# Performance work log

Hardware: AMD Instinct MI355X
Metric: run time of the kernel (lower is better)

Reference implementation:

```python
import jax, jax.numpy as jnp
import numpy as np

NUM_HEADS = 8


def setup_inputs() -> dict:
    key = jax.random.key(0)
    ks = jax.random.split(key, 7)
    b, t, prompt_dim, emb_dim = 2, 4096, 256, 512
    hidden = emb_dim  # head_dim=None -> hidden_dim = emb_dim
    def xavier(k, fan_in, fan_out):
        limit = np.sqrt(6.0 / (fan_in + fan_out)).astype(np.float32)
        return jax.random.uniform(k, (fan_in, fan_out), jnp.float32, -limit, limit)
    return {
        "prompt": jax.random.normal(ks[0], (b, t, prompt_dim), jnp.float32),
        "Wp": xavier(ks[1], prompt_dim, emb_dim),
        "bp": jnp.zeros((emb_dim,), jnp.float32),
        "Wqkv": xavier(ks[2], emb_dim, 3 * hidden),
        "bqkv": jnp.zeros((3 * hidden,), jnp.float32),
        "Wo": xavier(ks[3], hidden, prompt_dim),
        "bo": jnp.zeros((prompt_dim,), jnp.float32),
    }


def reference(prompt, Wp, bp, Wqkv, bqkv, Wo, bo):
    # prompt_proj
    x = prompt @ Wp + bp                      # [b, t, emb_dim]
    b, t, c = x.shape
    qkv = x @ Wqkv + bqkv                     # [b, t, 3*hidden]
    q, k, v = jnp.split(qkv, 3, axis=2)
    def to_heads(z):
        return z.reshape(b, t, NUM_HEADS, -1).transpose(0, 2, 1, 3)  # [b, h, t, d]
    q, k, v = to_heads(q), to_heads(k), to_heads(v)
    d = k.shape[-1]
    scores = jnp.einsum("bhid,bhjd->bhij", q, k) / jnp.sqrt(jnp.float32(d))
    attn = jax.nn.softmax(scores, axis=-1)    # dropout = identity (eval)
    out = jnp.einsum("bhij,bhjd->bhid", attn, v)
    out = out.transpose(0, 2, 1, 3).reshape(b, t, -1)  # [b, t, hidden]
    return out @ Wo + bo                      # [b, t, prompt_dim]
```

## Files before the change

### kernel.cpp

```cpp
#include <hip/hip_runtime.h>
#include <math.h>
#include <stdint.h>


typedef unsigned short u16;
typedef __attribute__((ext_vector_type(8))) __bf16 bf16x8;
typedef __attribute__((ext_vector_type(4))) __bf16 bf16x4;
typedef __attribute__((ext_vector_type(4))) float f32x4;

#define AS1 __attribute__((address_space(1)))
#define AS3 __attribute__((address_space(3)))

__device__ __forceinline__ void async16(const void* g, void* l) {
  __builtin_amdgcn_global_load_lds((const AS1 void*)g, (AS3 void*)l, 16, 0, 0);
}

__device__ __forceinline__ u16 f2bf(float f) {
  union { float f; unsigned u; } c; c.f = f;
  return (u16)((c.u + 0x7fffu + ((c.u >> 16) & 1u)) >> 16);
}

__global__ void prep_kernel(const float* __restrict__ prompt, u16* __restrict__ pbf,
                            const float* __restrict__ Wp, const float* __restrict__ Wqkv,
                            const float* __restrict__ Wo, u16* __restrict__ woT,
                            const float* __restrict__ bp, const float* __restrict__ bqkv,
                            float* __restrict__ bfused, u16* __restrict__ wfT) {
  __shared__ u16 Asf[64 * 40];
  __shared__ u16 Bsf[64 * 32];
  __shared__ float red[256];
  const int bid = blockIdx.x, tid = threadIdx.x;
  if (bid < 96) {
    const int k0 = (bid & 3) * 64, n0 = (bid >> 2) * 64;
    const int lane = tid & 63, w = tid >> 6;
    const int wr = w >> 1, wc = w & 1;
    const int lr = lane >> 4, lc = lane & 15;
    f32x4 acc[2][2];
#pragma unroll
    for (int a = 0; a < 2; a++)
#pragma unroll
      for (int b = 0; b < 2; b++) acc[a][b] = (f32x4){0.f, 0.f, 0.f, 0.f};
    for (int e0 = 0; e0 < 512; e0 += 32) {
      {
        const int er = tid >> 3, ng = (tid & 7) * 8;
        float4 v1 = *(const float4*)&Wqkv[(e0 + er) * 1536 + n0 + ng];
        float4 v2 = *(const float4*)&Wqkv[(e0 + er) * 1536 + n0 + ng + 4];
        Asf[(ng + 0) * 40 + er] = f2bf(v1.x); Asf[(ng + 1) * 40 + er] = f2bf(v1.y);
        Asf[(ng + 2) * 40 + er] = f2bf(v1.z); Asf[(ng + 3) * 40 + er] = f2bf(v1.w);
        Asf[(ng + 4) * 40 + er] = f2bf(v2.x); Asf[(ng + 5) * 40 + er] = f2bf(v2.y);
        Asf[(ng + 6) * 40 + er] = f2bf(v2.z); Asf[(ng + 7) * 40 + er] = f2bf(v2.w);
      }
      {
        const int kr = tid >> 2, ec = (tid & 3) * 8;
        float4 w1 = *(const float4*)&Wp[(k0 + kr) * 512 + e0 + ec];
        float4 w2 = *(const float4*)&Wp[(k0 + kr) * 512 + e0 + ec + 4];
        u16 tmp[8] = {f2bf(w1.x), f2bf(w1.y), f2bf(w1.z), f2bf(w1.w),
                      f2bf(w2.x), f2bf(w2.y), f2bf(w2.z), f2bf(w2.w)};
        *(uint4*)&Bsf[kr * 32 + ec] = *(const uint4*)&tmp[0];
      }
      __syncthreads();
      bf16x8 af[2], bf2[2];
#pragma unroll
      for (int mi = 0; mi < 2; mi++)
        af[mi] = *(const bf16x8*)&Asf[(wr * 32 + mi * 16 + lc) * 40 + lr * 8];
#pragma unroll
      for (int nj = 0; nj < 2; nj++)
        bf2[nj] = *(const bf16x8*)&Bsf[(wc * 32 + nj * 16 + lc) * 32 + lr * 8];
#pragma unroll
      for (int mi = 0; mi < 2; mi++)
#pragma unroll
        for (int nj = 0; nj < 2; nj++)
          acc[mi][nj] = __builtin_amdgcn_mfma_f32_16x16x32_bf16(af[mi], bf2[nj], acc[mi][nj], 0, 0, 0);
      __syncthreads();
    }
#pragma unroll
    for (int mi = 0; mi < 2; mi++)
#pragma unroll
      for (int nj = 0; nj < 2; nj++)
#pragma unroll
        for (int r = 0; r < 4; r++)
          wfT[(n0 + wr * 32 + mi * 16 + 4 * lr + r) * 256 + k0 + wc * 32 + nj * 16 + lc] =
              f2bf(acc[mi][nj][r]);
  } else if (bid < 120) {
    const int nloc = tid & 63, slice = tid >> 6;
    const int n = (bid - 96) * 64 + nloc;
    float s = 0.f;
#pragma unroll 8
    for (int e = slice * 128; e < slice * 128 + 128; e++) s += bp[e] * Wqkv[e * 1536 + n];
    red[tid] = s;
    __syncthreads();
    if (slice == 0)
      bfused[n] = red[nloc] + red[64 + nloc] + red[128 + nloc] + red[192 + nloc] + bqkv[n];
  } else if (bid < 632) {
    int j = (bid - 120) * 256 + tid;
    int n = j >> 9, k = j & 511;
    woT[j] = f2bf(Wo[k * 256 + n]);
  } else {
    int i = (bid - 632) * 256 + tid;
    float4 v = ((const float4*)prompt)[i];
    ushort4 o;
    o.x = f2bf(v.x); o.y = f2bf(v.y); o.z = f2bf(v.z); o.w = f2bf(v.w);
    ((ushort4*)pbf)[i] = o;
  }
}

__global__ __launch_bounds__(256) void gemm_qkv(
    const u16* __restrict__ A, const u16* __restrict__ Bt, const float* __restrict__ bias,
    u16* __restrict__ qO, u16* __restrict__ kO, u16* __restrict__ vO, int K) {
  constexpr int TM = 128, MI = 4, NJ = 4;
  __shared__ __align__(16) u16 As[2][TM * 32];
  __shared__ __align__(16) u16 Bs[2][TM * 32];
  const int tid = threadIdx.x;
  const int lane = tid & 63, w = tid >> 6;
  const int wr = w >> 1, wc = w & 1;
  const int lr = lane >> 4, lc = lane & 15;
  const long tileM = (long)blockIdx.y * 128;
  const long tileN = (long)blockIdx.x * 128;

  f32x4 acc[MI][NJ];
#pragma unroll
  for (int a = 0; a < MI; a++)
#pragma unroll
    for (int b = 0; b < NJ; b++) acc[a][b] = (f32x4){0.f, 0.f, 0.f, 0.f};

  const int r0 = lane >> 2;
  const int blk = lane & 3;

  auto stage = [&](int buf, int k0) {
#pragma unroll
    for (int i = 0; i < 2; i++) {
      int r = w * 32 + i * 16 + r0;
      int g = (blk ^ ((r >> 1) & 3)) << 3;
      async16(A + (tileM + r) * (long)K + k0 + g, (void*)&As[buf][(w * 32 + i * 16) * 32]);
      async16(Bt + (tileN + r) * (long)K + k0 + g, (void*)&Bs[buf][(w * 32 + i * 16) * 32]);
    }
  };

  stage(0, 0);
  for (int k0 = 0; k0 < K; k0 += 32) {
    const int cur = (k0 >> 5) & 1;
    stage(cur ^ 1, (k0 + 32 < K) ? k0 + 32 : 0);
    asm volatile("s_waitcnt vmcnt(4)" ::: "memory");
    asm volatile("s_barrier" ::: "memory");

    bf16x8 af[MI], bfv[NJ];
#pragma unroll
    for (int mi = 0; mi < MI; mi++) {
      int r = wr * 64 + mi * 16 + lc;
      af[mi] = *(const bf16x8*)&As[cur][r * 32 + ((lr ^ ((r >> 1) & 3)) << 3)];
    }
#pragma unroll
    for (int nj = 0; nj < NJ; nj++) {
      int r = wc * 64 + nj * 16 + lc;
      bfv[nj] = *(const bf16x8*)&Bs[cur][r * 32 + ((lr ^ ((r >> 1) & 3)) << 3)];
    }
#pragma unroll
    for (int mi = 0; mi < MI; mi++)
#pragma unroll
      for (int nj = 0; nj < NJ; nj++)
        acc[mi][nj] = __builtin_amdgcn_mfma_f32_16x16x32_bf16(af[mi], bfv[nj], acc[mi][nj], 0, 0, 0);
    asm volatile("s_barrier" ::: "memory");
  }

#pragma unroll
  for (int mi = 0; mi < MI; mi++)
#pragma unroll
    for (int nj = 0; nj < NJ; nj++) {
      long col = tileN + wc * 64 + nj * 16 + lc;
      float bcol = bias[col];
      long row0 = tileM + wr * 64 + mi * 16 + lr * 4;
      int sec = (int)(col >> 9);
      int c2 = (int)(col & 511);
      int h = c2 >> 6, d = c2 & 63;
      long pl = (row0 >> 12) * 8 + h;
      long t0 = row0 & 4095;
      if (sec == 2) {
        ushort4 pk;
        pk.x = f2bf(acc[mi][nj][0] + bcol);
        pk.y = f2bf(acc[mi][nj][1] + bcol);
        pk.z = f2bf(acc[mi][nj][2] + bcol);
        pk.w = f2bf(acc[mi][nj][3] + bcol);
        *(ushort4*)&vO[(pl * 64 + d) * 4096 + t0] = pk;
      } else {
        u16* dst = sec ? kO : qO;
        const float sc = sec ? 1.f : 0.18033688f;
#pragma unroll
        for (int r = 0; r < 4; r++)
          dst[((pl * 4096 + t0 + r) << 6) + d] = f2bf((acc[mi][nj][r] + bcol) * sc);
      }
    }
}

__global__ __launch_bounds__(512) void flash_attn(
    const u16* __restrict__ Q, const u16* __restrict__ Kg,
    const u16* __restrict__ VTg, u16* __restrict__ Op, float* __restrict__ lp) {
  __shared__ __align__(16) u16 KV[2][8192];
  __shared__ __align__(16) u16 Ps[8 * 2048];

  const int tid = threadIdx.x, lane = tid & 63, w = tid >> 6;
  const int lr = lane >> 4, lc = lane & 15;
  const int plane = blockIdx.y;
  const int split = blockIdx.z;
  const long pbase = (long)plane << 18;
  const int qr0 = blockIdx.x * 256 + w * 32;
  const int tj0 = split * 32;

  bf16x8 bq[2][2];
#pragma unroll
  for (int qi = 0; qi < 2; qi++)
#pragma unroll
    for (int kk = 0; kk < 2; kk++)
      bq[qi][kk] = *(const bf16x8*)&Q[pbase + (long)(qr0 + qi * 16 + lc) * 64 + kk * 32 + lr * 8];

  bf16x8 ones;
#pragma unroll
  for (int u = 0; u < 8; u++) ones[u] = (__bf16)1.0f;

  f32x4 o[2][4], o1[2];
#pragma unroll
  for (int mi = 0; mi < 2; mi++) {
    o1[mi] = (f32x4){0.f, 0.f, 0.f, 0.f};
#pragma unroll
    for (int nj = 0; nj < 4; nj++) o[mi][nj] = (f32x4){0.f, 0.f, 0.f, 0.f};
  }

  const int krow = lane >> 3, kblk = lane & 7;

  auto stage = [&](int buf, int tj) {
    const u16* kS = Kg + pbase + (long)tj * 4096;
    const u16* vS = VTg + pbase + (long)tj * 64;
    int row = w * 8 + krow;
    async16(kS + (long)row * 64 + ((kblk ^ (row & 7)) << 3),
            (void*)&KV[buf][(w * 8) * 64]);
    async16(vS + (long)row * 4096 + ((kblk ^ (row & 7)) << 3),
            (void*)&KV[buf][4096 + (w * 8) * 64]);
  };

  stage(0, tj0);
  for (int j = 0; j < 32; j++) {
    const int cur = j & 1;
    stage(cur ^ 1, (j + 1 < 32) ? tj0 + j + 1 : tj0);
    asm volatile("s_waitcnt vmcnt(2)" ::: "memory");
    asm volatile("s_barrier" ::: "memory");

    const u16* Ks = &KV[cur][0];
    const u16* Vt = &KV[cur][4096];

    f32x4 s[4][2];
#pragma unroll
    for (int ki = 0; ki < 4; ki++)
#pragma unroll
      for (int qi = 0; qi < 2; qi++) s[ki][qi] = (f32x4){0.f, 0.f, 0.f, 0.f};
#pragma unroll
    for (int ki = 0; ki < 4; ki++) {
      const int row = ki * 16 + lc;
      bf16x8 ak[2];
#pragma unroll
      for (int kk = 0; kk < 2; kk++)
        ak[kk] = *(const bf16x8*)&Ks[row * 64 + (((kk * 4 + lr) ^ (row & 7)) << 3)];
#pragma unroll
      for (int qi = 0; qi < 2; qi++)
#pragma unroll
        for (int kk = 0; kk < 2; kk++)
          s[ki][qi] = __builtin_amdgcn_mfma_f32_16x16x32_bf16(ak[kk], bq[qi][kk], s[ki][qi], 0, 0, 0);
    }

#pragma unroll
    for (int qi = 0; qi < 2; qi++) {
      const int pb = w * 2048 + (qi * 16 + lc) * 64 + 4 * (lr & 1);
#pragma unroll
      for (int ki = 0; ki < 4; ki++) {
        bf16x4 pk;
        pk[0] = (__bf16)__builtin_amdgcn_exp2f(s[ki][qi][0]);
        pk[1] = (__bf16)__builtin_amdgcn_exp2f(s[ki][qi][1]);
        pk[2] = (__bf16)__builtin_amdgcn_exp2f(s[ki][qi][2]);
        pk[3] = (__bf16)__builtin_amdgcn_exp2f(s[ki][qi][3]);
        *(bf16x4*)&Ps[pb + (((2 * ki + (lr >> 1)) ^ (lc & 7)) << 3)] = pk;
      }
    }

#pragma unroll
    for (int kk = 0; kk < 2; kk++) {
      bf16x8 ap[2];
#pragma unroll
      for (int mi = 0; mi < 2; mi++)
        ap[mi] = *(const bf16x8*)&Ps[w * 2048 + (mi * 16 + lc) * 64 + (((kk * 4 + lr) ^ (lc & 7)) << 3)];
#pragma unroll
      for (int nj = 0; nj < 4; nj++) {
        const int row = nj * 16 + lc;
        bf16x8 bv = *(const bf16x8*)&Vt[row * 64 + (((kk * 4 + lr) ^ (row & 7)) << 3)];
#pragma unroll
        for (int mi = 0; mi < 2; mi++)
          o[mi][nj] = __builtin_amdgcn_mfma_f32_16x16x32_bf16(ap[mi], bv, o[mi][nj], 0, 0, 0);
      }
#pragma unroll
      for (int mi = 0; mi < 2; mi++)
        o1[mi] = __builtin_amdgcn_mfma_f32_16x16x32_bf16(ap[mi], ones, o1[mi], 0, 0, 0);
    }
    asm volatile("s_barrier" ::: "memory");
  }

  const int bb = plane >> 3, h = plane & 7;
  u16* Ob = Op + (long)split * 4194304;
#pragma unroll
  for (int mi = 0; mi < 2; mi++)
#pragma unroll
    for (int r = 0; r < 4; r++) {
      long t = qr0 + mi * 16 + 4 * lr + r;
#pragma unroll
      for (int nj = 0; nj < 4; nj++)
        Ob[(((long)(bb * 4096 + t) * 8 + h) << 6) + nj * 16 + lc] = f2bf(o[mi][nj][r]);
      if (lc == 0) lp[((split * 16 + plane) << 12) + t] = o1[mi][r];
    }
}

__global__ __launch_bounds__(256) void gemm_out(
    const u16* __restrict__ Op, const float* __restrict__ lp,
    const u16* __restrict__ Bt, const float* __restrict__ bias,
    float* __restrict__ outf) {
  constexpr int K = 512;
  __shared__ __align__(16) u16 As[2][64 * 32];
  __shared__ __align__(16) u16 Bs[2][64 * 32];
  const int tid = threadIdx.x;
  const int lane = tid & 63, w = tid >> 6;
  const int wr = w >> 1, wc = w & 1;
  const int lr = lane >> 4, lc = lane & 15;
  const long tileM = (long)blockIdx.y * 64;
  const long tileN = (long)blockIdx.x * 64;

  f32x4 acc[2][2];
#pragma unroll
  for (int a = 0; a < 2; a++)
#pragma unroll
    for (int b = 0; b < 2; b++) acc[a][b] = (f32x4){0.f, 0.f, 0.f, 0.f};

  const int r0 = lane >> 2;
  const int blk = lane & 3;

  auto stageB = [&](int buf, int k0) {
    int r = w * 16 + r0;
    int g = (blk ^ ((r >> 1) & 3)) << 3;
    async16(Bt + (tileN + r) * (long)K + k0 + g, (void*)&Bs[buf][(w * 16) * 32]);
  };

  const int ar = tid >> 2, ablk = tid & 3;
  const long arow = tileM + ar;
  const int ab = (int)(arow >> 12), at = (int)(arow & 4095);

  auto stageA = [&](int buf, int k0) {
    int h = k0 >> 6;
    float l0 = lp[(long)((ab * 8 + h) << 12) + at];
    float l1 = lp[(long)((16 * 4096 * 4) + 0) + 0];
    (void)l1;
    float l = l0 + lp[(long)(((16 + ab * 8 + h)) << 12) + at];
    float inv = 1.f / l;
    long idx = arow * 512 + k0 + ablk * 8;
    bf16x8 v0 = *(const bf16x8*)&Op[idx];
    bf16x8 v1 = *(const bf16x8*)&Op[4194304 + idx];
    u16 tmp[8];
#pragma unroll
    for (int e = 0; e < 8; e++)
      tmp[e] = f2bf(((float)v0[e] + (float)v1[e]) * inv);
    *(uint4*)&As[buf][ar * 32 + ((ablk ^ ((ar >> 1) & 3)) << 3)] = *(const uint4*)&tmp[0];
  };

  stageB(0, 0);
  for (int k0 = 0; k0 < K; k0 += 32) {
    const int cur = (k0 >> 5) & 1;
    stageB(cur ^ 1, (k0 + 32 < K) ? k0 + 32 : 0);
    stageA(cur, k0);
    asm volatile("s_waitcnt vmcnt(1) lgkmcnt(0)" ::: "memory");
    asm volatile("s_barrier" ::: "memory");

    bf16x8 af[2], bfv[2];
#pragma unroll
    for (int mi = 0; mi < 2; mi++) {
      int r = wr * 32 + mi * 16 + lc;
      af[mi] = *(const bf16x8*)&As[cur][r * 32 + ((lr ^ ((r >> 1) & 3)) << 3)];
    }
#pragma unroll
    for (int nj = 0; nj < 2; nj++) {
      int r = wc * 32 + nj * 16 + lc;
      bfv[nj] = *(const bf16x8*)&Bs[cur][r * 32 + ((lr ^ ((r >> 1) & 3)) << 3)];
    }
#pragma unroll
    for (int mi = 0; mi < 2; mi++)
#pragma unroll
      for (int nj = 0; nj < 2; nj++)
        acc[mi][nj] = __builtin_amdgcn_mfma_f32_16x16x32_bf16(af[mi], bfv[nj], acc[mi][nj], 0, 0, 0);
    asm volatile("s_barrier" ::: "memory");
  }

#pragma unroll
  for (int mi = 0; mi < 2; mi++)
#pragma unroll
    for (int nj = 0; nj < 2; nj++) {
      long col = tileN + wc * 32 + nj * 16 + lc;
      float bcol = bias[col];
      long row0 = tileM + wr * 32 + mi * 16 + lr * 4;
#pragma unroll
      for (int r = 0; r < 4; r++)
        outf[(row0 + r) * 256 + col] = acc[mi][nj][r] + bcol;
    }
}

extern "C" void kernel_launch(void* const* d_in, const int* in_sizes, int n_in,
                              void* d_out, int out_size, void* d_ws, size_t ws_size,
                              hipStream_t stream) {
  const float* prompt = (const float*)d_in[0];
  const float* Wp = (const float*)d_in[1];
  const float* bp = (const float*)d_in[2];
  const float* Wqkv = (const float*)d_in[3];
  const float* bqkv = (const float*)d_in[4];
  const float* Wo = (const float*)d_in[5];
  const float* bo = (const float*)d_in[6];
  float* out = (float*)d_out;

  char* ws = (char*)d_ws;
  const size_t MiB = 1024 * 1024;
  u16* qb     = (u16*)(ws + 0);
  u16* kb     = (u16*)(ws + 8 * MiB);
  u16* vb     = (u16*)(ws + 16 * MiB);
  u16* pbf    = (u16*)(ws + 24 * MiB);
  float* lpp  = (float*)(ws + 24 * MiB);
  u16* Op     = (u16*)(ws + 28 * MiB);
  u16* woT    = (u16*)(ws + 44 * MiB);
  u16* wfT    = (u16*)(ws + 44 * MiB + 256 * 1024);
  float* bfused = (float*)(ws + 45 * MiB);

  prep_kernel<<<dim3(2680), dim3(256), 0, stream>>>(
      prompt, pbf, Wp, Wqkv, Wo, woT, bp, bqkv, bfused, wfT);

  gemm_qkv<<<dim3(12, 64), dim3(256), 0, stream>>>(
      pbf, wfT, bfused, qb, kb, vb, 256);

  flash_attn<<<dim3(16, 16, 2), dim3(512), 0, stream>>>(qb, kb, vb, Op, lpp);

  gemm_out<<<dim3(4, 128), dim3(256), 0, stream>>>(Op, lpp, woT, bo, out);
}
```

Measured before the change: 187.9 us.

## Keep softmax P in registers by permuting V layout, halve attention query tile

The QKV GEMM now writes V^T with a permuted time order, so the exp2 results of the QK^T MFMA can be packed straight into the A operand of the PV MFMA. This removes the shared-memory round trip for P. Each wave now handles 16 queries instead of 32, and the grid doubles, with a remapped block index that groups planes and splits together. The goal is to cut LDS traffic and shared-memory footprint to raise occupancy, at the cost of reusing each K/V tile over fewer queries.

```diff
diff --git a/kernel.cpp b/kernel.cpp
--- a/kernel.cpp
+++ b/kernel.cpp
@@ -179,7 +179,10 @@
         pk.y = f2bf(acc[mi][nj][1] + bcol);
         pk.z = f2bf(acc[mi][nj][2] + bcol);
         pk.w = f2bf(acc[mi][nj][3] + bcol);
-        *(ushort4*)&vO[(pl * 64 + d) * 4096 + t0] = pk;
+        int g = (int)((t0 >> 2) & 7);
+        int posg = ((g & 3) << 1) | (g >> 2);
+        long tp = (t0 & ~31L) | (posg << 2);
+        *(ushort4*)&vO[(pl * 64 + d) * 4096 + tp] = pk;
       } else {
         u16* dst = sec ? kO : qO;
         const float sc = sec ? 1.f : 0.18033688f;
@@ -190,38 +193,35 @@
     }
 }
 
-__global__ __launch_bounds__(512) void flash_attn(
+__global__ __launch_bounds__(512, 8) void flash_attn(
     const u16* __restrict__ Q, const u16* __restrict__ Kg,
     const u16* __restrict__ VTg, u16* __restrict__ Op, float* __restrict__ lp) {
   __shared__ __align__(16) u16 KV[2][8192];
-  __shared__ __align__(16) u16 Ps[8 * 2048];
 
   const int tid = threadIdx.x, lane = tid & 63, w = tid >> 6;
+  const int linear = blockIdx.x + 32 * (blockIdx.y + 16 * blockIdx.z);
+  const int qt = linear >> 5;
+  const int g = linear & 31;
+  const int plane = g & 15;
+  const int split = g >> 4;
   const int lr = lane >> 4, lc = lane & 15;
-  const int plane = blockIdx.y;
-  const int split = blockIdx.z;
   const long pbase = (long)plane << 18;
-  const int qr0 = blockIdx.x * 256 + w * 32;
+  const int qr0 = qt * 128 + w * 16;
   const int tj0 = split * 32;
 
-  bf16x8 bq[2][2];
-#pragma unroll
-  for (int qi = 0; qi < 2; qi++)
-#pragma unroll
-    for (int kk = 0; kk < 2; kk++)
-      bq[qi][kk] = *(const bf16x8*)&Q[pbase + (long)(qr0 + qi * 16 + lc) * 64 + kk * 32 + lr * 8];
+  bf16x8 bq[2];
+#pragma unroll
+  for (int kk = 0; kk < 2; kk++)
+    bq[kk] = *(const bf16x8*)&Q[pbase + (long)(qr0 + lc) * 64 + kk * 32 + lr * 8];
 
   bf16x8 ones;
 #pragma unroll
   for (int u = 0; u < 8; u++) ones[u] = (__bf16)1.0f;
 
-  f32x4 o[2][4], o1[2];
-#pragma unroll
-  for (int mi = 0; mi < 2; mi++) {
-    o1[mi] = (f32x4){0.f, 0.f, 0.f, 0.f};
-#pragma unroll
-    for (int nj = 0; nj < 4; nj++) o[mi][nj] = (f32x4){0.f, 0.f, 0.f, 0.f};
-  }
+  f32x4 o[4], o1;
+  o1 = (f32x4){0.f, 0.f, 0.f, 0.f};
+#pragma unroll
+  for (int nj = 0; nj < 4; nj++) o[nj] = (f32x4){0.f, 0.f, 0.f, 0.f};
 
   const int krow = lane >> 3, kblk = lane & 7;
 
@@ -245,56 +245,35 @@
     const u16* Ks = &KV[cur][0];
     const u16* Vt = &KV[cur][4096];
 
-    f32x4 s[4][2];
-#pragma unroll
-    for (int ki = 0; ki < 4; ki++)
-#pragma unroll
-      for (int qi = 0; qi < 2; qi++) s[ki][qi] = (f32x4){0.f, 0.f, 0.f, 0.f};
+    f32x4 s[4];
+#pragma unroll
+    for (int ki = 0; ki < 4; ki++) s[ki] = (f32x4){0.f, 0.f, 0.f, 0.f};
 #pragma unroll
     for (int ki = 0; ki < 4; ki++) {
       const int row = ki * 16 + lc;
-      bf16x8 ak[2];
-#pragma unroll
-      for (int kk = 0; kk < 2; kk++)
-        ak[kk] = *(const bf16x8*)&Ks[row * 64 + (((kk * 4 + lr) ^ (row & 7)) << 3)];
-#pragma unroll
-      for (int qi = 0; qi < 2; qi++)
-#pragma unroll
-        for (int kk = 0; kk < 2; kk++)
-          s[ki][qi] = __builtin_amdgcn_mfma_f32_16x16x32_bf16(ak[kk], bq[qi][kk], s[ki][qi], 0, 0, 0);
-    }
-
-#pragma unroll
-    for (int qi = 0; qi < 2; qi++) {
-      const int pb = w * 2048 + (qi * 16 + lc) * 64 + 4 * (lr & 1);
-#pragma unroll
-      for (int ki = 0; ki < 4; ki++) {
-        bf16x4 pk;
-        pk[0] = (__bf16)__builtin_amdgcn_exp2f(s[ki][qi][0]);
-        pk[1] = (__bf16)__builtin_amdgcn_exp2f(s[ki][qi][1]);
-        pk[2] = (__bf16)__builtin_amdgcn_exp2f(s[ki][qi][2]);
-        pk[3] = (__bf16)__builtin_amdgcn_exp2f(s[ki][qi][3]);
-        *(bf16x4*)&Ps[pb + (((2 * ki + (lr >> 1)) ^ (lc & 7)) << 3)] = pk;
+#pragma unroll
+      for (int kk = 0; kk < 2; kk++) {
+        bf16x8 ak = *(const bf16x8*)&Ks[row * 64 + (((kk * 4 + lr) ^ (row & 7)) << 3)];
+        s[ki] = __builtin_amdgcn_mfma_f32_16x16x32_bf16(ak, bq[kk], s[ki], 0, 0, 0);
       }
     }
 
 #pragma unroll
     for (int kk = 0; kk < 2; kk++) {
-      bf16x8 ap[2];
-#pragma unroll
-      for (int mi = 0; mi < 2; mi++)
-        ap[mi] = *(const bf16x8*)&Ps[w * 2048 + (mi * 16 + lc) * 64 + (((kk * 4 + lr) ^ (lc & 7)) << 3)];
+      union { u16 s2[8]; bf16x8 v; } pf;
+#pragma unroll
+      for (int r = 0; r < 4; r++) {
+        pf.s2[r]     = f2bf(__builtin_amdgcn_exp2f(s[2 * kk][r]));
+        pf.s2[4 + r] = f2bf(__builtin_amdgcn_exp2f(s[2 * kk + 1][r]));
+      }
+      const bf16x8 ap = pf.v;
 #pragma unroll
       for (int nj = 0; nj < 4; nj++) {
         const int row = nj * 16 + lc;
         bf16x8 bv = *(const bf16x8*)&Vt[row * 64 + (((kk * 4 + lr) ^ (row & 7)) << 3)];
-#pragma unroll
-        for (int mi = 0; mi < 2; mi++)
-          o[mi][nj] = __builtin_amdgcn_mfma_f32_16x16x32_bf16(ap[mi], bv, o[mi][nj], 0, 0, 0);
-      }
-#pragma unroll
-      for (int mi = 0; mi < 2; mi++)
-        o1[mi] = __builtin_amdgcn_mfma_f32_16x16x32_bf16(ap[mi], ones, o1[mi], 0, 0, 0);
+        o[nj] = __builtin_amdgcn_mfma_f32_16x16x32_bf16(ap, bv, o[nj], 0, 0, 0);
+      }
+      o1 = __builtin_amdgcn_mfma_f32_16x16x32_bf16(ap, ones, o1, 0, 0, 0);
     }
     asm volatile("s_barrier" ::: "memory");
   }
@@ -302,15 +281,13 @@
   const int bb = plane >> 3, h = plane & 7;
   u16* Ob = Op + (long)split * 4194304;
 #pragma unroll
-  for (int mi = 0; mi < 2; mi++)
-#pragma unroll
-    for (int r = 0; r < 4; r++) {
-      long t = qr0 + mi * 16 + 4 * lr + r;
-#pragma unroll
-      for (int nj = 0; nj < 4; nj++)
-        Ob[(((long)(bb * 4096 + t) * 8 + h) << 6) + nj * 16 + lc] = f2bf(o[mi][nj][r]);
-      if (lc == 0) lp[((split * 16 + plane) << 12) + t] = o1[mi][r];
-    }
+  for (int r = 0; r < 4; r++) {
+    long t = qr0 + 4 * lr + r;
+#pragma unroll
+    for (int nj = 0; nj < 4; nj++)
+      Ob[(((long)(bb * 4096 + t) * 8 + h) << 6) + nj * 16 + lc] = f2bf(o[nj][r]);
+    if (lc == 0) lp[((split * 16 + plane) << 12) + t] = o1[r];
+  }
 }
 
 __global__ __launch_bounds__(256) void gemm_out(
@@ -348,10 +325,8 @@
 
   auto stageA = [&](int buf, int k0) {
     int h = k0 >> 6;
-    float l0 = lp[(long)((ab * 8 + h) << 12) + at];
-    float l1 = lp[(long)((16 * 4096 * 4) + 0) + 0];
-    (void)l1;
-    float l = l0 + lp[(long)(((16 + ab * 8 + h)) << 12) + at];
+    float l = lp[(long)((ab * 8 + h) << 12) + at] +
+              lp[(long)((16 + ab * 8 + h) << 12) + at];
     float inv = 1.f / l;
     long idx = arow * 512 + k0 + ablk * 8;
     bf16x8 v0 = *(const bf16x8*)&Op[idx];
@@ -433,7 +408,7 @@
   gemm_qkv<<<dim3(12, 64), dim3(256), 0, stream>>>(
       pbf, wfT, bfused, qb, kb, vb, 256);
 
-  flash_attn<<<dim3(16, 16, 2), dim3(512), 0, stream>>>(qb, kb, vb, Op, lpp);
+  flash_attn<<<dim3(32, 16, 2), dim3(512), 0, stream>>>(qb, kb, vb, Op, lpp);
 
   gemm_out<<<dim3(4, 128), dim3(256), 0, stream>>>(Op, lpp, woT, bo, out);
 }
```

Result: slower. 198.5 us (+5.6%).

## Keep softmax P in registers by permuting V layout; remap attention grid

Applied to the files above, without the earlier changes.

The attention kernel no longer writes exp2 scores to a shared-memory P buffer and reads them back. Instead the S accumulator registers are fed directly as the A operand of the PV MFMA. To make this work, the QKV epilogue stores V^T with a permuted token order inside each 32-token group, so the register layout of P matches V's k ordering. The change also remaps the block index so that consecutive blocks cover different planes and splits, adds a launch-bounds occupancy hint, and removes a dead lp load. It saves LDS traffic and barriers but depends on the permutation exactly matching the MFMA operand layout.

```diff
diff --git a/kernel.cpp b/kernel.cpp
--- a/kernel.cpp
+++ b/kernel.cpp
@@ -179,7 +179,10 @@
         pk.y = f2bf(acc[mi][nj][1] + bcol);
         pk.z = f2bf(acc[mi][nj][2] + bcol);
         pk.w = f2bf(acc[mi][nj][3] + bcol);
-        *(ushort4*)&vO[(pl * 64 + d) * 4096 + t0] = pk;
+        int g = (int)((t0 >> 2) & 7);
+        int posg = ((g & 3) << 1) | (g >> 2);
+        long tp = (t0 & ~31L) | (posg << 2);
+        *(ushort4*)&vO[(pl * 64 + d) * 4096 + tp] = pk;
       } else {
         u16* dst = sec ? kO : qO;
         const float sc = sec ? 1.f : 0.18033688f;
@@ -190,18 +193,20 @@
     }
 }
 
-__global__ __launch_bounds__(512) void flash_attn(
+__global__ __launch_bounds__(512, 4) void flash_attn(
     const u16* __restrict__ Q, const u16* __restrict__ Kg,
     const u16* __restrict__ VTg, u16* __restrict__ Op, float* __restrict__ lp) {
   __shared__ __align__(16) u16 KV[2][8192];
-  __shared__ __align__(16) u16 Ps[8 * 2048];
 
   const int tid = threadIdx.x, lane = tid & 63, w = tid >> 6;
+  const int linear = blockIdx.x + 16 * (blockIdx.y + 16 * blockIdx.z);
+  const int qt = linear >> 5;
+  const int g = linear & 31;
+  const int plane = g & 15;
+  const int split = g >> 4;
   const int lr = lane >> 4, lc = lane & 15;
-  const int plane = blockIdx.y;
-  const int split = blockIdx.z;
   const long pbase = (long)plane << 18;
-  const int qr0 = blockIdx.x * 256 + w * 32;
+  const int qr0 = qt * 256 + w * 32;
   const int tj0 = split * 32;
 
   bf16x8 bq[2][2];
@@ -214,13 +219,14 @@
   bf16x8 ones;
 #pragma unroll
   for (int u = 0; u < 8; u++) ones[u] = (__bf16)1.0f;
+  const f32x4 zero4 = (f32x4){0.f, 0.f, 0.f, 0.f};
 
   f32x4 o[2][4], o1[2];
 #pragma unroll
   for (int mi = 0; mi < 2; mi++) {
-    o1[mi] = (f32x4){0.f, 0.f, 0.f, 0.f};
-#pragma unroll
-    for (int nj = 0; nj < 4; nj++) o[mi][nj] = (f32x4){0.f, 0.f, 0.f, 0.f};
+    o1[mi] = zero4;
+#pragma unroll
+    for (int nj = 0; nj < 4; nj++) o[mi][nj] = zero4;
   }
 
   const int krow = lane >> 3, kblk = lane & 7;
@@ -247,10 +253,6 @@
 
     f32x4 s[4][2];
 #pragma unroll
-    for (int ki = 0; ki < 4; ki++)
-#pragma unroll
-      for (int qi = 0; qi < 2; qi++) s[ki][qi] = (f32x4){0.f, 0.f, 0.f, 0.f};
-#pragma unroll
     for (int ki = 0; ki < 4; ki++) {
       const int row = ki * 16 + lc;
       bf16x8 ak[2];
@@ -258,23 +260,9 @@
       for (int kk = 0; kk < 2; kk++)
         ak[kk] = *(const bf16x8*)&Ks[row * 64 + (((kk * 4 + lr) ^ (row & 7)) << 3)];
 #pragma unroll
-      for (int qi = 0; qi < 2; qi++)
-#pragma unroll
-        for (int kk = 0; kk < 2; kk++)
-          s[ki][qi] = __builtin_amdgcn_mfma_f32_16x16x32_bf16(ak[kk], bq[qi][kk], s[ki][qi], 0, 0, 0);
-    }
-
-#pragma unroll
-    for (int qi = 0; qi < 2; qi++) {
-      const int pb = w * 2048 + (qi * 16 + lc) * 64 + 4 * (lr & 1);
-#pragma unroll
-      for (int ki = 0; ki < 4; ki++) {
-        bf16x4 pk;
-        pk[0] = (__bf16)__builtin_amdgcn_exp2f(s[ki][qi][0]);
-        pk[1] = (__bf16)__builtin_amdgcn_exp2f(s[ki][qi][1]);
-        pk[2] = (__bf16)__builtin_amdgcn_exp2f(s[ki][qi][2]);
-        pk[3] = (__bf16)__builtin_amdgcn_exp2f(s[ki][qi][3]);
-        *(bf16x4*)&Ps[pb + (((2 * ki + (lr >> 1)) ^ (lc & 7)) << 3)] = pk;
+      for (int qi = 0; qi < 2; qi++) {
+        s[ki][qi] = __builtin_amdgcn_mfma_f32_16x16x32_bf16(ak[0], bq[qi][0], zero4, 0, 0, 0);
+        s[ki][qi] = __builtin_amdgcn_mfma_f32_16x16x32_bf16(ak[1], bq[qi][1], s[ki][qi], 0, 0, 0);
       }
     }
 
@@ -282,8 +270,15 @@
     for (int kk = 0; kk < 2; kk++) {
       bf16x8 ap[2];
 #pragma unroll
-      for (int mi = 0; mi < 2; mi++)
-        ap[mi] = *(const bf16x8*)&Ps[w * 2048 + (mi * 16 + lc) * 64 + (((kk * 4 + lr) ^ (lc & 7)) << 3)];
+      for (int qi = 0; qi < 2; qi++) {
+        bf16x8 p;
+#pragma unroll
+        for (int r = 0; r < 4; r++) {
+          p[r]     = (__bf16)__builtin_amdgcn_exp2f(s[2 * kk][qi][r]);
+          p[4 + r] = (__bf16)__builtin_amdgcn_exp2f(s[2 * kk + 1][qi][r]);
+        }
+        ap[qi] = p;
+      }
 #pragma unroll
       for (int nj = 0; nj < 4; nj++) {
         const int row = nj * 16 + lc;
@@ -348,10 +343,8 @@
 
   auto stageA = [&](int buf, int k0) {
     int h = k0 >> 6;
-    float l0 = lp[(long)((ab * 8 + h) << 12) + at];
-    float l1 = lp[(long)((16 * 4096 * 4) + 0) + 0];
-    (void)l1;
-    float l = l0 + lp[(long)(((16 + ab * 8 + h)) << 12) + at];
+    float l = lp[(long)((ab * 8 + h) << 12) + at] +
+              lp[(long)((16 + ab * 8 + h) << 12) + at];
     float inv = 1.f / l;
     long idx = arow * 512 + k0 + ablk * 8;
     bf16x8 v0 = *(const bf16x8*)&Op[idx];
```

New measurement: 176.5 us. 6.0% less time.
